# Kernel tuning notes

Measured on AMD Instinct MI355X. Metric: run time of the kernel, lower is better.

## Reference

```python
import jax, jax.numpy as jnp
import numpy as np
import math

HEADS = 8
GROUPS = 4
PW = 2  # pooling_window
EPS = 1e-5


def group_norm(x, w, b, groups=GROUPS):
    # x: (B, C, *spatial); normalize over (C//groups, *spatial) per group
    B, C = x.shape[0], x.shape[1]
    xs = x.reshape(B, groups, -1)
    mu = xs.mean(-1, keepdims=True)
    var = xs.var(-1, keepdims=True)
    xs = (xs - mu) / jnp.sqrt(var + EPS)
    shape = (1, C) + (1,) * (x.ndim - 2)
    return xs.reshape(x.shape) * w.reshape(shape) + b.reshape(shape)


def cst_pool(x, pw=PW):
    # x: (B, C, Tq, Ts) with Ts = h*w + 1 (class token first); avg-pool spatial part
    cls_tok, sp = x[..., :1], x[..., 1:]
    B, C, Tq, S = sp.shape
    h = math.isqrt(S)
    sp = sp.reshape(B, C, Tq, h // pw, pw, h // pw, pw).mean(axis=(4, 6))
    return jnp.concatenate([cls_tok, sp.reshape(B, C, Tq, -1)], axis=-1)


def conv1x1(x, w):
    # w: (O, C); x: (B, C, Tq, Ts)
    return jnp.einsum('oc,bcqs->boqs', w, x)


def interp_bilinear_ac(m, n):
    # bilinear resize to (n, n), align_corners=True; m: (B, H, W) float
    def axis_interp(x, size, axis, L):
        c = jnp.linspace(0.0, L - 1.0, size)
        i0 = jnp.floor(c).astype(jnp.int32)
        i1 = jnp.minimum(i0 + 1, L - 1)
        f = (c - i0).astype(x.dtype)
        x0 = jnp.take(x, i0, axis=axis)
        x1 = jnp.take(x, i1, axis=axis)
        shape = [1] * x.ndim
        shape[axis] = size
        f = f.reshape(shape)
        return x0 * (1 - f) + x1 * f
    B, H, W = m.shape
    return axis_interp(axis_interp(m, n, 1, H), n, 2, W)


def setup_inputs() -> dict:
    key = jax.random.key(0)
    ks = jax.random.split(key, 8)
    B, Cin, Tq, Ts = 4, 128, 256, 257
    Cout = 512
    hidden = Cout // 2  # 256
    H = W = 256
    s = 0.05
    return {
        'corr_tokens': jax.random.normal(ks[0], (B, Cin, Tq, Ts), jnp.float32),
        's_masks': jax.random.randint(ks[1], (B, H, W), 0, 2, jnp.int32),
        'W_sc': jax.random.normal(ks[2], (Cout, Cin), jnp.float32) * s,
        'gn_sc_w': jnp.ones((Cout,), jnp.float32),
        'gn_sc_b': jnp.zeros((Cout,), jnp.float32),
        'W_qkv': jax.random.normal(ks[3], (3 * hidden, Cin), jnp.float32) * s,
        'b_qkv': jax.random.normal(ks[4], (3 * hidden,), jnp.float32) * s,
        'gn1_w': jnp.ones((hidden,), jnp.float32),
        'gn1_b': jnp.zeros((hidden,), jnp.float32),
        'W_agg': jax.random.normal(ks[5], (Cout, hidden), jnp.float32) * s,
        'gn2_w': jnp.ones((Cout,), jnp.float32),
        'gn2_b': jnp.zeros((Cout,), jnp.float32),
        'gn_out_w': jnp.ones((Cout,), jnp.float32),
        'gn_out_b': jnp.zeros((Cout,), jnp.float32),
    }


def reference(corr_tokens, s_masks, W_sc, gn_sc_w, gn_sc_b, W_qkv, b_qkv,
              gn1_w, gn1_b, W_agg, gn2_w, gn2_b, gn_out_w, gn_out_b):
    B, _, Tq, Ts = corr_tokens.shape
    hidden = W_qkv.shape[0] // 3
    E = hidden // HEADS

    # short_cut branch: conv1x1 -> CSTPooling -> GroupNorm -> ReLU
    residual = jax.nn.relu(group_norm(cst_pool(conv1x1(corr_tokens, W_sc)), gn_sc_w, gn_sc_b))

    # qkv projection
    qkv = conv1x1(corr_tokens, W_qkv) + b_qkv[None, :, None, None]
    qkv = qkv.reshape(B, 3, HEADS, E, Tq, Ts)  # channel order (x, g, e)
    q, k, v = qkv[:, 0], qkv[:, 1], qkv[:, 2]

    # pool queries over support-spatial dim: (B,G,E,Tq,Ts) -> (B,G,E,Tq,Td)
    q = cst_pool(q.reshape(B, hidden, Tq, Ts))
    Td = q.shape[-1]
    q = q.reshape(B, HEADS, E, Tq, Td)

    # per-query masked attention
    attn = jnp.einsum('bgeqd,bgeqs->bgqds', q, k)  # (B,G,Tq,Td,Ts)
    sdim = math.isqrt(Ts - 1)
    m = interp_bilinear_ac(jnp.minimum(s_masks, 1).astype(jnp.float32), sdim)
    m = m.reshape(B, 1, 1, 1, sdim * sdim)
    attn_seg = jnp.where(m == 0, jnp.float32(-1e9), attn[..., 1:])
    attn = jnp.concatenate([attn[..., :1], attn_seg], axis=-1)
    attn = jax.nn.softmax(attn, axis=-1)
    out = jnp.einsum('bgqds,bgeqs->bgeqd', attn, v).reshape(B, hidden, Tq, Td)

    # agg: GN -> ReLU -> conv1x1 -> GN -> ReLU
    out = jax.nn.relu(group_norm(out, gn1_w, gn1_b))
    out = conv1x1(out, W_agg)
    out = jax.nn.relu(group_norm(out, gn2_w, gn2_b))

    return group_norm(out + residual, gn_out_w, gn_out_b)
```

## Files before the change

### kernel.cpp

```cpp
#include <hip/hip_runtime.h>
#include <stdint.h>

#define NB    4
#define TQ    256
#define TS    257
#define TD    65
#define NPIX  16640
#define NPADQ 264
#define NPAD  67584
#define COUT  512
#define HID   256

typedef __attribute__((ext_vector_type(8))) short bf16x8;
typedef __attribute__((ext_vector_type(4))) float f32x4;

__device__ __forceinline__ float bf2f(unsigned short u) {
    union { unsigned int i; float f; } v; v.i = ((unsigned int)u) << 16; return v.f;
}
__device__ __forceinline__ unsigned short f2bf(float x) {
    union { float f; unsigned int i; } v; v.f = x;
    unsigned int r = v.i + 0x7fffu + ((v.i >> 16) & 1u);
    return (unsigned short)(r >> 16);
}

__device__ __forceinline__ float2 gn_params(const float* st, int bg, float invcnt) {
    float mu  = st[bg * 2] * invcnt;
    float var = st[bg * 2 + 1] * invcnt - mu * mu;
    float2 r; r.x = mu; r.y = rsqrtf(var + 1e-5f); return r;
}

__device__ __forceinline__ void gld_lds16(const void* g, void* l) {
    __builtin_amdgcn_global_load_lds(
        (const __attribute__((address_space(1))) unsigned int*)(size_t)g,
        (__attribute__((address_space(3))) unsigned int*)(unsigned int)(size_t)l,
        16, 0, 0);
}

__global__ void wprep_kernel(const float* __restrict__ wq, const float* __restrict__ wsc,
                             const float* __restrict__ wagg, unsigned short* __restrict__ wb) {
    int i = blockIdx.x * 256 + threadIdx.x;
    float v;
    if (i < 98304) v = wq[i];
    else if (i < 163840) v = wsc[i - 98304];
    else v = wagg[i - 163840];
    wb[i] = f2bf(v);
}

__global__ void mask_kernel(const int* __restrict__ sm, float* __restrict__ bias) {
    int b = blockIdx.x; int t = threadIdx.x;
    if (t >= 272) return;
    float v;
    if (t == 0) v = 0.0f;
    else if (t <= 256) {
        int s = t - 1; int i = s >> 4, j = s & 15;
        v = (sm[(size_t)b * 65536 + i * 17 * 256 + j * 17] != 0) ? 0.0f : -1e9f;
    } else v = -1e9f;
    bias[b * 272 + t] = v;
}

__global__ __launch_bounds__(256) void tpool_kernel(
    const float* __restrict__ corr,
    unsigned short* __restrict__ corrT,
    unsigned short* __restrict__ corrpT)
{
    int q = blockIdx.x, ch = blockIdx.y, b = blockIdx.z;
    int t = threadIdx.x;
    __shared__ unsigned short sT[264 * 66];

    {
        int laneT = t & 63; int crow = t >> 6;
        for (int c = crow; c < 64; c += 4) {
            const float* src = corr + (((size_t)b * 128 + ch * 64 + c) * 256 + q) * 257;
            for (int s = laneT; s < 257; s += 64) sT[s * 66 + c] = f2bf(src[s]);
        }
    }
    for (int idx = t; idx < 7 * 66; idx += 256) {
        int s = 257 + idx / 66, c = idx % 66;
        sT[s * 66 + c] = 0;
    }
    __syncthreads();

    {
        unsigned int* dst = (unsigned int*)corrT;
        size_t base = (size_t)b * (NPAD * 64) + (size_t)q * (264 * 64) + ch * 32;
        for (int idx = t; idx < 264 * 32; idx += 256) {
            int s = idx >> 5, cu = idx & 31;
            unsigned int v = (unsigned int)sT[s * 66 + 2 * cu] |
                             ((unsigned int)sT[s * 66 + 2 * cu + 1] << 16);
            dst[base + (size_t)s * 64 + cu] = v;
        }
    }
    {
        unsigned int* dst = (unsigned int*)corrpT;
        size_t base = (size_t)b * (NPIX * 64) + (size_t)q * (65 * 64) + ch * 32;
        for (int idx = t; idx < 65 * 32; idx += 256) {
            int d = idx >> 5, cu = idx & 31;
            float x0, x1;
            if (d == 0) {
                x0 = bf2f(sT[0 * 66 + 2 * cu]); x1 = bf2f(sT[0 * 66 + 2 * cu + 1]);
            } else {
                int dd = d - 1; int i = dd >> 3, j = dd & 7;
                int s = 1 + i * 32 + j * 2;
                int c0 = 2 * cu, c1 = 2 * cu + 1;
                x0 = 0.25f * (bf2f(sT[s*66+c0]) + bf2f(sT[(s+1)*66+c0]) +
                              bf2f(sT[(s+16)*66+c0]) + bf2f(sT[(s+17)*66+c0]));
                x1 = 0.25f * (bf2f(sT[s*66+c1]) + bf2f(sT[(s+1)*66+c1]) +
                              bf2f(sT[(s+16)*66+c1]) + bf2f(sT[(s+17)*66+c1]));
            }
            unsigned int v = (unsigned int)f2bf(x0) | ((unsigned int)f2bf(x1) << 16);
            dst[base + (size_t)d * 64 + cu] = v;
        }
    }
}

template<int MODE, int KT>
__global__ __launch_bounds__(256) void mgemm_kernel(
    const unsigned short* __restrict__ X,
    const unsigned short* __restrict__ Wb,
    int Nn,
    float* __restrict__ Yf,
    unsigned short* __restrict__ Y16,
    unsigned short* __restrict__ kb,
    unsigned short* __restrict__ vb,
    const float* __restrict__ bias,
    const float* __restrict__ st, const float* __restrict__ gw, const float* __restrict__ gb,
    float invcnt)
{
    int b  = blockIdx.z;
    int n0 = blockIdx.x * 128;
    int m0 = blockIdx.y * 128;
    int t = threadIdx.x;
    int w = t >> 6, lane = t & 63;
    int lm = lane & 15, lg = lane >> 4;
    int wn = (w & 1) * 64, wm = (w >> 1) * 64;

    __shared__ __align__(16) unsigned short sX[16384];
    __shared__ __align__(16) unsigned short sW[16384];

    f32x4 acc[4][4];
    #pragma unroll
    for (int i = 0; i < 4; i++)
        #pragma unroll
        for (int j = 0; j < 4; j++) { acc[i][j][0]=0.f; acc[i][j][1]=0.f; acc[i][j][2]=0.f; acc[i][j][3]=0.f; }

    for (int kc = 0; kc < KT / 128; kc++) {
        for (int i = t; i < 2048; i += 256) {
            int r_ = i >> 4, kq = i & 15;
            uint4 xv = *(const uint4*)&X[((size_t)b * Nn + n0 + r_) * KT + kc * 128 + (kq << 3)];
            if (MODE == 3) {
                union { uint4 v; unsigned short us[8]; } u; u.v = xv;
                int c0 = kc * 128 + (kq << 3);
                float2 p = gn_params(st, b * 4 + (c0 >> 6), invcnt);
                #pragma unroll
                for (int jj = 0; jj < 8; jj++) {
                    int cc = c0 + jj;
                    float v = bf2f(u.us[jj]);
                    v = fmaxf((v - p.x) * p.y * gw[cc] + gb[cc], 0.0f);
                    u.us[jj] = f2bf(v);
                }
                xv = u.v;
            }
            *(uint4*)&sX[r_ * 128 + ((kq ^ (r_ & 15)) << 3)] = xv;
            uint4 wv = *(const uint4*)&Wb[((size_t)(m0 + r_)) * KT + kc * 128 + (kq << 3)];
            *(uint4*)&sW[r_ * 128 + ((kq ^ (r_ & 15)) << 3)] = wv;
        }
        __syncthreads();
        #pragma unroll
        for (int kk = 0; kk < 4; kk++) {
            int kg = (kk << 2) | lg;
            bf16x8 af[4], bw[4];
            #pragma unroll
            for (int ii = 0; ii < 4; ii++)
                af[ii] = *(const bf16x8*)&sX[(wn + ii * 16 + lm) * 128 + ((kg ^ lm) << 3)];
            #pragma unroll
            for (int jj = 0; jj < 4; jj++)
                bw[jj] = *(const bf16x8*)&sW[(wm + jj * 16 + lm) * 128 + ((kg ^ lm) << 3)];
            #pragma unroll
            for (int ii = 0; ii < 4; ii++)
                #pragma unroll
                for (int jj = 0; jj < 4; jj++) {
                    if (MODE == 0)
                        acc[ii][jj] = __builtin_amdgcn_mfma_f32_16x16x32_bf16(bw[jj], af[ii], acc[ii][jj], 0,0,0);
                    else
                        acc[ii][jj] = __builtin_amdgcn_mfma_f32_16x16x32_bf16(af[ii], bw[jj], acc[ii][jj], 0,0,0);
                }
        }
        __syncthreads();
    }

    if (MODE == 0) {
        #pragma unroll
        for (int ii = 0; ii < 4; ii++) {
            int n = n0 + wn + ii * 16 + lm;
            #pragma unroll
            for (int jj = 0; jj < 4; jj++) {
                int mb = m0 + wm + jj * 16 + lg * 4;
                union { unsigned short us[4]; uint2 v; } pk;
                #pragma unroll
                for (int r = 0; r < 4; r++) pk.us[r] = f2bf(acc[ii][jj][r] + bias[mb + r]);
                *(uint2*)&Y16[((size_t)b * NPIX + n) * 256 + mb] = pk.v;
            }
        }
    } else if (MODE == 1) {
        if (m0 < 256) {
            #pragma unroll
            for (int ii = 0; ii < 4; ii++) {
                #pragma unroll
                for (int r = 0; r < 4; r++) {
                    unsigned int np = (unsigned int)(n0 + wn + ii * 16 + lg * 4 + r);
                    unsigned int qq = np / 264u;
                    unsigned int s  = np - qq * 264u;
                    #pragma unroll
                    for (int jj = 0; jj < 4; jj++) {
                        int m = m0 + wm + jj * 16 + lm;
                        int gch = m >> 5, e = m & 31;
                        kb[(((size_t)(b * 8 + gch) * 256 + qq) * 264 + s) * 32 + e] =
                            f2bf(acc[ii][jj][r] + bias[m]);
                    }
                }
            }
        } else {
            #pragma unroll
            for (int ii = 0; ii < 4; ii++) {
                int nb = n0 + wn + ii * 16 + lg * 4;
                #pragma unroll
                for (int jj = 0; jj < 4; jj++) {
                    int m = m0 + wm + jj * 16 + lm;
                    int mv = m - 256;
                    union { unsigned short us[4]; uint2 v; } pk;
                    #pragma unroll
                    for (int r = 0; r < 4; r++) pk.us[r] = f2bf(acc[ii][jj][r] + bias[m]);
                    *(uint2*)&vb[((size_t)b * 256 + mv) * NPAD + nb] = pk.v;
                }
            }
        }
    } else {
        #pragma unroll
        for (int ii = 0; ii < 4; ii++) {
            int nb = n0 + wn + ii * 16 + lg * 4;
            #pragma unroll
            for (int jj = 0; jj < 4; jj++) {
                int m = m0 + wm + jj * 16 + lm;
                *(f32x4*)&Yf[((size_t)b * COUT + m) * NPIX + nb] = acc[ii][jj];
            }
        }
    }
}

__global__ __launch_bounds__(320, 3) void attn_kernel(
    const unsigned short* __restrict__ kb,
    const unsigned short* __restrict__ vb,
    const unsigned short* __restrict__ qpT,
    const unsigned short* __restrict__ zpad,
    const float* __restrict__ bias272,
    unsigned short* __restrict__ attT)
{
    int g = blockIdx.x, q = blockIdx.y, b = blockIdx.z;
    int t = threadIdx.x;
    int w = t >> 6, lane = t & 63;
    int lm = lane & 15, lg = lane >> 4;

    __shared__ __align__(16) unsigned short sbuf[17920];
    const int VB = 8704;

    int d = w * 16 + lm;
    int dc = d < 64 ? d : 64;
    bf16x8 qa = *(const bf16x8*)&qpT[((size_t)b * NPIX + q * 65 + dc) * 256 + g * 32 + lg * 8];
    if (d >= TD) { bf16x8 z = {}; qa = z; }

    size_t kb0 = ((size_t)(b * 8 + g) * 256 + q) * (264 * 32);
    size_t vrow0 = (size_t)b * 256 + g * 32;
    for (int cc = w; cc < 35; cc += 5) {
        unsigned o = cc * 1024 + lane * 16;
        const unsigned short* src;
        if (cc < 17) {
            unsigned mr = o >> 8, sl = (o >> 4) & 15;
            unsigned lam = (o & ~0xF0u) | ((sl ^ (mr & 15)) << 4);
            src = (lam < 16896u) ? (kb + kb0 + (lam >> 1)) : zpad;
        } else {
            unsigned ov = o - 17408u;
            unsigned mr = ov >> 8, sl = (ov >> 4) & 15;
            unsigned lam = (ov & ~0xF0u) | ((sl ^ (mr & 15)) << 4);
            unsigned kk = lam >> 11, ch = (lam >> 6) & 31;
            unsigned s = kk * 32 + ((lam >> 4) & 3) * 8;
            src = (s < 264u) ? (vb + ((vrow0 + ch) * NPAD + (size_t)q * 264 + s)) : zpad;
        }
        gld_lds16(src, &sbuf[cc * 512]);
    }
    asm volatile("s_waitcnt vmcnt(0)" ::: "memory");
    __syncthreads();

    f32x4 zero4 = {0.f, 0.f, 0.f, 0.f};
    f32x4 c[17];
    int sl0 = ((lm & 3) << 2) | lg;
    #pragma unroll
    for (int tt = 0; tt < 17; tt++) {
        int mr = tt * 4 + (lm >> 2);
        bf16x8 kf = *(const bf16x8*)&sbuf[mr * 128 + ((sl0 ^ (mr & 15)) << 3)];
        c[tt] = __builtin_amdgcn_mfma_f32_16x16x32_bf16(kf, qa, zero4, 0, 0, 0);
    }

    const float* bp = bias272 + b * 272 + lg * 4;
    #pragma unroll
    for (int tt = 0; tt < 17; tt++) {
        f32x4 bf = *(const f32x4*)&bp[tt * 16];
        c[tt][0] += bf[0]; c[tt][1] += bf[1]; c[tt][2] += bf[2]; c[tt][3] += bf[3];
    }

    f32x4 mv = c[0];
    #pragma unroll
    for (int tt = 1; tt < 17; tt++) {
        mv[0] = fmaxf(mv[0], c[tt][0]); mv[1] = fmaxf(mv[1], c[tt][1]);
        mv[2] = fmaxf(mv[2], c[tt][2]); mv[3] = fmaxf(mv[3], c[tt][3]);
    }
    float mx = fmaxf(fmaxf(mv[0], mv[1]), fmaxf(mv[2], mv[3]));
    mx = fmaxf(mx, __shfl_xor(mx, 16));
    mx = fmaxf(mx, __shfl_xor(mx, 32));
    float sm = 0.f;
    #pragma unroll
    for (int tt = 0; tt < 17; tt++) {
        #pragma unroll
        for (int r = 0; r < 4; r++) { float e_ = __expf(c[tt][r] - mx); c[tt][r] = e_; sm += e_; }
    }
    sm += __shfl_xor(sm, 16);
    sm += __shfl_xor(sm, 32);
    float inv = 1.0f / sm;

    unsigned plo[17], phi[17];
    #pragma unroll
    for (int tt = 0; tt < 17; tt++) {
        asm("v_cvt_pk_bf16_f32 %0, %1, %2" : "=v"(plo[tt]) : "v"(c[tt][0]), "v"(c[tt][1]));
        asm("v_cvt_pk_bf16_f32 %0, %1, %2" : "=v"(phi[tt]) : "v"(c[tt][2]), "v"(c[tt][3]));
    }

    bool lgEven = (lane & 16) == 0;
    f32x4 o0 = zero4, o1 = zero4;
    #pragma unroll
    for (int kk = 0; kk < 9; kk++) {
        unsigned A = plo[2 * kk];
        unsigned C = phi[2 * kk];
        unsigned B = (2 * kk + 1 < 17) ? plo[2 * kk + 1] : 0u;
        unsigned D = (2 * kk + 1 < 17) ? phi[2 * kk + 1] : 0u;
        asm("v_permlane32_swap_b32 %0, %1" : "+v"(A), "+v"(B));
        asm("v_permlane32_swap_b32 %0, %1" : "+v"(C), "+v"(D));
        unsigned Ax = __shfl_xor(A, 16), Bx = __shfl_xor(B, 16);
        unsigned Cx = __shfl_xor(C, 16), Dx = __shfl_xor(D, 16);
        union { unsigned u[4]; bf16x8 v; } pa;
        pa.u[0] = lgEven ? A  : Bx;
        pa.u[1] = lgEven ? C  : Dx;
        pa.u[2] = lgEven ? Ax : B;
        pa.u[3] = lgEven ? Cx : D;
        int mr0 = kk * 8 + (lm >> 2), mr1 = mr0 + 4;
        bf16x8 v0 = *(const bf16x8*)&sbuf[VB + mr0 * 128 + ((sl0 ^ (mr0 & 15)) << 3)];
        bf16x8 v1 = *(const bf16x8*)&sbuf[VB + mr1 * 128 + ((sl0 ^ (mr1 & 15)) << 3)];
        o0 = __builtin_amdgcn_mfma_f32_16x16x32_bf16(pa.v, v0, o0, 0, 0, 0);
        o1 = __builtin_amdgcn_mfma_f32_16x16x32_bf16(pa.v, v1, o1, 0, 0, 0);
    }
    float invr[4];
    #pragma unroll
    for (int r = 0; r < 4; r++) invr[r] = __shfl(inv, lg * 4 + r);
    #pragma unroll
    for (int r = 0; r < 4; r++) {
        int dd = w * 16 + lg * 4 + r;
        if (dd < TD) {
            size_t nn = (size_t)b * NPIX + q * 65 + dd;
            attT[nn * 256 + g * 32 + lm]      = f2bf(o0[r] * invr[r]);
            attT[nn * 256 + g * 32 + 16 + lm] = f2bf(o1[r] * invr[r]);
        }
    }
}

__global__ void stats1_kernel(const unsigned short* __restrict__ attT, float* __restrict__ st) {
    int b = blockIdx.y;
    int t = threadIdx.x;
    int e8 = t & 31, g = e8 >> 3;
    int lane = t & 63;
    float s = 0.f, ss = 0.f;
    for (int r = blockIdx.x * 8 + (t >> 5); r < NPIX; r += gridDim.x * 8) {
        union { uint4 v; unsigned short us[8]; } u;
        u.v = *(const uint4*)&attT[((size_t)b * NPIX + r) * 256 + e8 * 8];
        #pragma unroll
        for (int j = 0; j < 8; j++) { float x = bf2f(u.us[j]); s += x; ss += x * x; }
    }
    s += __shfl_down(s, 32); ss += __shfl_down(ss, 32);
    s += __shfl_down(s, 4);  ss += __shfl_down(ss, 4);
    s += __shfl_down(s, 2);  ss += __shfl_down(ss, 2);
    s += __shfl_down(s, 1);  ss += __shfl_down(ss, 1);
    if (lane < 32 && (lane & 7) == 0) {
        atomicAdd(&st[(b * 4 + g) * 2],     s);
        atomicAdd(&st[(b * 4 + g) * 2 + 1], ss);
    }
}

__global__ void stats_kernel(const float* __restrict__ x, float* __restrict__ st, int Cg) {
    size_t len = (size_t)Cg * NPIX;
    size_t base = (size_t)blockIdx.y * len;
    const float4* x4 = reinterpret_cast<const float4*>(x + base);
    size_t len4 = len >> 2;
    float s = 0.f, ss = 0.f;
    for (size_t i = (size_t)blockIdx.x * blockDim.x + threadIdx.x; i < len4;
         i += (size_t)gridDim.x * blockDim.x) {
        float4 v = x4[i];
        s  += v.x + v.y + v.z + v.w;
        ss += v.x * v.x + v.y * v.y + v.z * v.z + v.w * v.w;
    }
    #pragma unroll
    for (int o = 32; o > 0; o >>= 1) { s += __shfl_down(s, o, 64); ss += __shfl_down(ss, o, 64); }
    __shared__ float red[4][2];
    int wid = threadIdx.x >> 6, lane = threadIdx.x & 63;
    if (lane == 0) { red[wid][0] = s; red[wid][1] = ss; }
    __syncthreads();
    if (threadIdx.x == 0) {
        float S  = red[0][0] + red[1][0] + red[2][0] + red[3][0];
        float SS = red[0][1] + red[1][1] + red[2][1] + red[3][1];
        atomicAdd(&st[blockIdx.y * 2],     S);
        atomicAdd(&st[blockIdx.y * 2 + 1], SS);
    }
}

__global__ void z_kernel(float* __restrict__ out, const float* __restrict__ scr,
                         const float* __restrict__ st2, const float* __restrict__ stsc,
                         const float* __restrict__ g2w, const float* __restrict__ g2b,
                         const float* __restrict__ gsw, const float* __restrict__ gsb)
{
    const float invcnt = 1.0f / (128.0f * NPIX);
    size_t total4 = (size_t)NB * COUT * (NPIX / 4);
    float4* o4 = reinterpret_cast<float4*>(out);
    const float4* s4 = reinterpret_cast<const float4*>(scr);
    for (size_t i = (size_t)blockIdx.x * blockDim.x + threadIdx.x; i < total4;
         i += (size_t)gridDim.x * blockDim.x) {
        size_t flat = i * 4;
        int c = (int)((flat / NPIX) % COUT);
        int b = (int)(flat / ((size_t)COUT * NPIX));
        int bg = b * 4 + (c >> 7);
        float2 p2 = gn_params(st2,  bg, invcnt);
        float2 ps = gn_params(stsc, bg, invcnt);
        float w2 = g2w[c] * p2.y, b2 = g2b[c] - p2.x * p2.y * g2w[c];
        float wsc = gsw[c] * ps.y, bsc = gsb[c] - ps.x * ps.y * gsw[c];
        float4 a = o4[i], r = s4[i], z;
        z.x = fmaxf(a.x * w2 + b2, 0.f) + fmaxf(r.x * wsc + bsc, 0.f);
        z.y = fmaxf(a.y * w2 + b2, 0.f) + fmaxf(r.y * wsc + bsc, 0.f);
        z.z = fmaxf(a.z * w2 + b2, 0.f) + fmaxf(r.z * wsc + bsc, 0.f);
        z.w = fmaxf(a.w * w2 + b2, 0.f) + fmaxf(r.w * wsc + bsc, 0.f);
        o4[i] = z;
    }
}

__global__ void norm_kernel(float* __restrict__ out, const float* __restrict__ st3,
                            const float* __restrict__ gw, const float* __restrict__ gb)
{
    const float invcnt = 1.0f / (128.0f * NPIX);
    size_t total4 = (size_t)NB * COUT * (NPIX / 4);
    float4* o4 = reinterpret_cast<float4*>(out);
    for (size_t i = (size_t)blockIdx.x * blockDim.x + threadIdx.x; i < total4;
         i += (size_t)gridDim.x * blockDim.x) {
        size_t flat = i * 4;
        int c = (int)((flat / NPIX) % COUT);
        int b = (int)(flat / ((size_t)COUT * NPIX));
        int bg = b * 4 + (c >> 7);
        float2 p = gn_params(st3, bg, invcnt);
        float w_ = gw[c] * p.y, b_ = gb[c] - p.x * p.y * gw[c];
        float4 a = o4[i], z;
        z.x = a.x * w_ + b_; z.y = a.y * w_ + b_; z.z = a.z * w_ + b_; z.w = a.w * w_ + b_;
        o4[i] = z;
    }
}

extern "C" void kernel_launch(void* const* d_in, const int* in_sizes, int n_in,
                              void* d_out, int out_size, void* d_ws, size_t ws_size,
                              hipStream_t stream) {
    (void)in_sizes; (void)n_in; (void)out_size; (void)ws_size;
    const float* corr     = (const float*)d_in[0];
    const int*   smask    = (const int*)  d_in[1];
    const float* W_sc     = (const float*)d_in[2];
    const float* gn_sc_w  = (const float*)d_in[3];
    const float* gn_sc_b  = (const float*)d_in[4];
    const float* W_qkv    = (const float*)d_in[5];
    const float* b_qkv    = (const float*)d_in[6];
    const float* gn1_w    = (const float*)d_in[7];
    const float* gn1_b    = (const float*)d_in[8];
    const float* W_agg    = (const float*)d_in[9];
    const float* gn2_w    = (const float*)d_in[10];
    const float* gn2_b    = (const float*)d_in[11];
    const float* gn_out_w = (const float*)d_in[12];
    const float* gn_out_b = (const float*)d_in[13];
    float* out = (float*)d_out;

    unsigned short* ws = (unsigned short*)d_ws;
    unsigned short* corrT  = ws;
    unsigned short* kbuf   = corrT  + (size_t)34603008;
    unsigned short* vbuf   = kbuf   + (size_t)69206016;
    unsigned short* corrpT = vbuf   + (size_t)69206016;
    unsigned short* qpT    = corrpT + (size_t)8519680;
    unsigned short* attT   = qpT    + (size_t)17039360;
    unsigned short* wbuf   = attT   + (size_t)17039360;
    float* bias  = (float*)(wbuf + (size_t)294912);
    float* stats = bias + 1088;
    float* scr   = (float*)d_ws;
    float* st_sc = stats, *st1 = stats + 32, *st2 = stats + 64, *st3 = stats + 96;

    const float inv1 = 1.0f / (64.0f * (float)NPIX);

    hipMemsetAsync(stats, 0, 128 * sizeof(float), stream);
    wprep_kernel<<<dim3(1152), dim3(256), 0, stream>>>(W_qkv, W_sc, W_agg, wbuf);
    mask_kernel<<<dim3(NB), dim3(320), 0, stream>>>(smask, bias);
    tpool_kernel<<<dim3(TQ, 2, NB), dim3(256), 0, stream>>>(corr, corrT, corrpT);
    mgemm_kernel<0,128><<<dim3(130, 2, NB), dim3(256), 0, stream>>>(
        corrpT, wbuf, NPIX, nullptr, qpT, nullptr, nullptr, b_qkv,
        nullptr, nullptr, nullptr, 0.f);
    mgemm_kernel<1,128><<<dim3(528, 4, NB), dim3(256), 0, stream>>>(
        corrT, wbuf + 32768, NPAD, nullptr, nullptr, kbuf, vbuf, b_qkv + 256,
        nullptr, nullptr, nullptr, 0.f);
    attn_kernel<<<dim3(8, TQ, NB), dim3(320), 0, stream>>>(
        kbuf, vbuf, qpT, corrT + 32896, bias, attT);
    stats1_kernel<<<dim3(208, NB), dim3(256), 0, stream>>>(attT, st1);
    mgemm_kernel<3,256><<<dim3(130, 4, NB), dim3(256), 0, stream>>>(
        attT, wbuf + 163840, NPIX, out, nullptr, nullptr, nullptr, nullptr,
        st1, gn1_w, gn1_b, inv1);
    stats_kernel<<<dim3(64, 16), dim3(256), 0, stream>>>(out, st2, 128);
    mgemm_kernel<2,128><<<dim3(130, 4, NB), dim3(256), 0, stream>>>(
        corrpT, wbuf + 98304, NPIX, scr, nullptr, nullptr, nullptr, nullptr,
        nullptr, nullptr, nullptr, 0.f);
    stats_kernel<<<dim3(64, 16), dim3(256), 0, stream>>>(scr, st_sc, 128);
    z_kernel<<<dim3(4096), dim3(256), 0, stream>>>(out, scr, st2, st_sc, gn2_w, gn2_b, gn_sc_w, gn_sc_b);
    stats_kernel<<<dim3(64, 16), dim3(256), 0, stream>>>(out, st3, 128);
    norm_kernel<<<dim3(4096), dim3(256), 0, stream>>>(out, st3, gn_out_w, gn_out_b);
}
```

Before: 982.4 us.

## Fuse K/V projection into attention kernel, dropping kbuf/vbuf materialization

Removes the separate MODE 1 GEMM that wrote K and V (bf16) to large global buffers, which the attention kernel then loaded back. The attention kernel now loads the per-query corrT tile and the K/V weight fragments and computes K and V with MFMA directly into swizzled LDS, adding bias and zero-padding in place. This removes a large global write and read of K/V. In exchange, each attention block reloads the 32-channel K/V weight slice and does the projection math itself, which adds register pressure and repeated weight loads, and it drops the async global-to-LDS load path.

New measurement: 970.7 us. About the same (-1.2%).

```diff
diff --git a/kernel.cpp b/kernel.cpp
--- a/kernel.cpp
+++ b/kernel.cpp
@@ -27,13 +27,6 @@
     float mu  = st[bg * 2] * invcnt;
     float var = st[bg * 2 + 1] * invcnt - mu * mu;
     float2 r; r.x = mu; r.y = rsqrtf(var + 1e-5f); return r;
-}
-
-__device__ __forceinline__ void gld_lds16(const void* g, void* l) {
-    __builtin_amdgcn_global_load_lds(
-        (const __attribute__((address_space(1))) unsigned int*)(size_t)g,
-        (__attribute__((address_space(3))) unsigned int*)(unsigned int)(size_t)l,
-        16, 0, 0);
 }
 
 __global__ void wprep_kernel(const float* __restrict__ wq, const float* __restrict__ wsc,
@@ -120,8 +113,6 @@
     int Nn,
     float* __restrict__ Yf,
     unsigned short* __restrict__ Y16,
-    unsigned short* __restrict__ kb,
-    unsigned short* __restrict__ vb,
     const float* __restrict__ bias,
     const float* __restrict__ st, const float* __restrict__ gw, const float* __restrict__ gb,
     float invcnt)
@@ -201,39 +192,6 @@
                 *(uint2*)&Y16[((size_t)b * NPIX + n) * 256 + mb] = pk.v;
             }
         }
-    } else if (MODE == 1) {
-        if (m0 < 256) {
-            #pragma unroll
-            for (int ii = 0; ii < 4; ii++) {
-                #pragma unroll
-                for (int r = 0; r < 4; r++) {
-                    unsigned int np = (unsigned int)(n0 + wn + ii * 16 + lg * 4 + r);
-                    unsigned int qq = np / 264u;
-                    unsigned int s  = np - qq * 264u;
-                    #pragma unroll
-                    for (int jj = 0; jj < 4; jj++) {
-                        int m = m0 + wm + jj * 16 + lm;
-                        int gch = m >> 5, e = m & 31;
-                        kb[(((size_t)(b * 8 + gch) * 256 + qq) * 264 + s) * 32 + e] =
-                            f2bf(acc[ii][jj][r] + bias[m]);
-                    }
-                }
-            }
-        } else {
-            #pragma unroll
-            for (int ii = 0; ii < 4; ii++) {
-                int nb = n0 + wn + ii * 16 + lg * 4;
-                #pragma unroll
-                for (int jj = 0; jj < 4; jj++) {
-                    int m = m0 + wm + jj * 16 + lm;
-                    int mv = m - 256;
-                    union { unsigned short us[4]; uint2 v; } pk;
-                    #pragma unroll
-                    for (int r = 0; r < 4; r++) pk.us[r] = f2bf(acc[ii][jj][r] + bias[m]);
-                    *(uint2*)&vb[((size_t)b * 256 + mv) * NPAD + nb] = pk.v;
-                }
-            }
-        }
     } else {
         #pragma unroll
         for (int ii = 0; ii < 4; ii++) {
@@ -248,10 +206,10 @@
 }
 
 __global__ __launch_bounds__(320, 3) void attn_kernel(
-    const unsigned short* __restrict__ kb,
-    const unsigned short* __restrict__ vb,
+    const unsigned short* __restrict__ corrT,
+    const unsigned short* __restrict__ wkv,
+    const float* __restrict__ bkv,
     const unsigned short* __restrict__ qpT,
-    const unsigned short* __restrict__ zpad,
     const float* __restrict__ bias272,
     unsigned short* __restrict__ attT)
 {
@@ -268,29 +226,80 @@
     bf16x8 qa = *(const bf16x8*)&qpT[((size_t)b * NPIX + q * 65 + dc) * 256 + g * 32 + lg * 8];
     if (d >= TD) { bf16x8 z = {}; qa = z; }
 
-    size_t kb0 = ((size_t)(b * 8 + g) * 256 + q) * (264 * 32);
-    size_t vrow0 = (size_t)b * 256 + g * 32;
-    for (int cc = w; cc < 35; cc += 5) {
-        unsigned o = cc * 1024 + lane * 16;
-        const unsigned short* src;
-        if (cc < 17) {
-            unsigned mr = o >> 8, sl = (o >> 4) & 15;
-            unsigned lam = (o & ~0xF0u) | ((sl ^ (mr & 15)) << 4);
-            src = (lam < 16896u) ? (kb + kb0 + (lam >> 1)) : zpad;
-        } else {
-            unsigned ov = o - 17408u;
-            unsigned mr = ov >> 8, sl = (ov >> 4) & 15;
-            unsigned lam = (ov & ~0xF0u) | ((sl ^ (mr & 15)) << 4);
-            unsigned kk = lam >> 11, ch = (lam >> 6) & 31;
-            unsigned s = kk * 32 + ((lam >> 4) & 3) * 8;
-            src = (s < 264u) ? (vb + ((vrow0 + ch) * NPAD + (size_t)q * 264 + s)) : zpad;
-        }
-        gld_lds16(src, &sbuf[cc * 512]);
-    }
-    asm volatile("s_waitcnt vmcnt(0)" ::: "memory");
+    bf16x8 wkf[2][4], wvf[2][4];
+    #pragma unroll
+    for (int et = 0; et < 2; et++)
+        #pragma unroll
+        for (int ks = 0; ks < 4; ks++) {
+            wkf[et][ks] = *(const bf16x8*)&wkv[(size_t)(g * 32 + et * 16 + lm) * 128 + ks * 32 + lg * 8];
+            wvf[et][ks] = *(const bf16x8*)&wkv[(size_t)(256 + g * 32 + et * 16 + lm) * 128 + ks * 32 + lg * 8];
+        }
+    float bk_[2][4], bv_[2];
+    #pragma unroll
+    for (int et = 0; et < 2; et++) {
+        #pragma unroll
+        for (int r = 0; r < 4; r++) bk_[et][r] = bkv[g * 32 + et * 16 + lg * 4 + r];
+        bv_[et] = bkv[256 + g * 32 + et * 16 + lm];
+    }
+
+    const unsigned short* cbase = corrT + ((size_t)b * NPAD + (size_t)q * 264) * 128;
+    f32x4 zero4 = {0.f, 0.f, 0.f, 0.f};
+
+    for (int st = w; st < 17; st += 5) {
+        int srow = st * 16 + lm; if (srow > 263) srow = 263;
+        bf16x8 ct[4];
+        #pragma unroll
+        for (int ks = 0; ks < 4; ks++)
+            ct[ks] = *(const bf16x8*)&cbase[(size_t)srow * 128 + ks * 32 + lg * 8];
+        f32x4 ak0 = zero4, ak1 = zero4, av0 = zero4, av1 = zero4;
+        #pragma unroll
+        for (int ks = 0; ks < 4; ks++) {
+            ak0 = __builtin_amdgcn_mfma_f32_16x16x32_bf16(wkf[0][ks], ct[ks], ak0, 0, 0, 0);
+            ak1 = __builtin_amdgcn_mfma_f32_16x16x32_bf16(wkf[1][ks], ct[ks], ak1, 0, 0, 0);
+            av0 = __builtin_amdgcn_mfma_f32_16x16x32_bf16(ct[ks], wvf[0][ks], av0, 0, 0, 0);
+            av1 = __builtin_amdgcn_mfma_f32_16x16x32_bf16(ct[ks], wvf[1][ks], av1, 0, 0, 0);
+        }
+        {
+            int s = st * 16 + lm;
+            #pragma unroll
+            for (int et = 0; et < 2; et++) {
+                unsigned u = (unsigned)(s * 64 + et * 32 + lg * 8);
+                unsigned mr = u >> 8, sl = (u >> 4) & 15;
+                unsigned us = (u & ~0xF0u) | ((sl ^ (mr & 15)) << 4);
+                union { unsigned short e[4]; uint2 v; } pk;
+                f32x4 a = et ? ak1 : ak0;
+                #pragma unroll
+                for (int r = 0; r < 4; r++) pk.e[r] = f2bf(a[r] + bk_[et][r]);
+                *(uint2*)((char*)sbuf + us) = pk.v;
+            }
+        }
+        {
+            int s0 = st * 16 + lg * 4;
+            unsigned vb_off = (unsigned)((s0 >> 5) * 2048 + (s0 & 31) * 2);
+            #pragma unroll
+            for (int et = 0; et < 2; et++) {
+                int ch = et * 16 + lm;
+                unsigned ov = vb_off + (unsigned)ch * 64u;
+                unsigned mr = ov >> 8, sl = (ov >> 4) & 15;
+                unsigned ovs = (ov & ~0xF0u) | ((sl ^ (mr & 15)) << 4);
+                union { unsigned short e[4]; uint2 v; } pk;
+                f32x4 a = et ? av1 : av0;
+                #pragma unroll
+                for (int r = 0; r < 4; r++) pk.e[r] = f2bf(a[r] + bv_[et]);
+                *(uint2*)((char*)sbuf + 17408 + ovs) = pk.v;
+            }
+        }
+    }
+    if (t < 128) {
+        int ch = t >> 2, j = t & 3;
+        unsigned ov = 16384u + (unsigned)ch * 64u + 32u + (unsigned)j * 8u;
+        unsigned mr = ov >> 8, sl = (ov >> 4) & 15;
+        unsigned ovs = (ov & ~0xF0u) | ((sl ^ (mr & 15)) << 4);
+        uint2 z2; z2.x = 0u; z2.y = 0u;
+        *(uint2*)((char*)sbuf + 17408 + ovs) = z2;
+    }
     __syncthreads();
 
-    f32x4 zero4 = {0.f, 0.f, 0.f, 0.f};
     f32x4 c[17];
     int sl0 = ((lm & 3) << 2) | lg;
     #pragma unroll
@@ -498,6 +507,7 @@
     float* stats = bias + 1088;
     float* scr   = (float*)d_ws;
     float* st_sc = stats, *st1 = stats + 32, *st2 = stats + 64, *st3 = stats + 96;
+    (void)kbuf; (void)vbuf;
 
     const float inv1 = 1.0f / (64.0f * (float)NPIX);
 
@@ -506,20 +516,17 @@
     mask_kernel<<<dim3(NB), dim3(320), 0, stream>>>(smask, bias);
     tpool_kernel<<<dim3(TQ, 2, NB), dim3(256), 0, stream>>>(corr, corrT, corrpT);
     mgemm_kernel<0,128><<<dim3(130, 2, NB), dim3(256), 0, stream>>>(
-        corrpT, wbuf, NPIX, nullptr, qpT, nullptr, nullptr, b_qkv,
-        nullptr, nullptr, nullptr, 0.f);
-    mgemm_kernel<1,128><<<dim3(528, 4, NB), dim3(256), 0, stream>>>(
-        corrT, wbuf + 32768, NPAD, nullptr, nullptr, kbuf, vbuf, b_qkv + 256,
+        corrpT, wbuf, NPIX, nullptr, qpT, b_qkv,
         nullptr, nullptr, nullptr, 0.f);
     attn_kernel<<<dim3(8, TQ, NB), dim3(320), 0, stream>>>(
-        kbuf, vbuf, qpT, corrT + 32896, bias, attT);
+        corrT, wbuf + 32768, b_qkv + 256, qpT, bias, attT);
     stats1_kernel<<<dim3(208, NB), dim3(256), 0, stream>>>(attT, st1);
     mgemm_kernel<3,256><<<dim3(130, 4, NB), dim3(256), 0, stream>>>(
-        attT, wbuf + 163840, NPIX, out, nullptr, nullptr, nullptr, nullptr,
+        attT, wbuf + 163840, NPIX, out, nullptr, nullptr,
         st1, gn1_w, gn1_b, inv1);
     stats_kernel<<<dim3(64, 16), dim3(256), 0, stream>>>(out, st2, 128);
     mgemm_kernel<2,128><<<dim3(130, 4, NB), dim3(256), 0, stream>>>(
-        corrpT, wbuf + 98304, NPIX, scr, nullptr, nullptr, nullptr, nullptr,
+        corrpT, wbuf + 98304, NPIX, scr, nullptr, nullptr,
         nullptr, nullptr, nullptr, 0.f);
     stats_kernel<<<dim3(64, 16), dim3(256), 0, stream>>>(scr, st_sc, 128);
     z_kernel<<<dim3(4096), dim3(256), 0, stream>>>(out, scr, st2, st_sc, gn2_w, gn2_b, gn_sc_w, gn_sc_b);
```
